# Performance work log

Measured on AMD Instinct MI355X. Metric: run time of the kernel, lower is better.

## Reference

```python
import jax, jax.numpy as jnp
import numpy as np

B, S, IN, EMB, H = 4, 2048, 256, 512, 8
D = EMB // H
SCALE = 1.0 / np.sqrt(EMB)  # source uses 1/sqrt(embed_size), not head_dim
EPS = 1e-5


def setup_inputs() -> dict:
    key = jax.random.key(0)
    ks = jax.random.split(key, 20)
    def w(k, shape, fan_in):
        return jax.random.normal(k, shape, jnp.float32) * (1.0 / np.sqrt(fan_in))
    inp = {"state_emb": jax.random.normal(ks[0], (B, S, IN), jnp.float32)}
    i = 1
    for p in ("q", "k", "v"):
        inp[f"{p}_W1"] = w(ks[i], (IN, EMB), IN); i += 1
        inp[f"{p}_b1"] = jnp.zeros((EMB,), jnp.float32)
        inp[f"{p}_W2"] = w(ks[i], (EMB, EMB), EMB); i += 1
        inp[f"{p}_b2"] = jnp.zeros((EMB,), jnp.float32)
    inp["f_W1"] = w(ks[i], (EMB, 2 * EMB), EMB); i += 1
    inp["f_b1"] = jnp.zeros((2 * EMB,), jnp.float32)
    inp["f_W2"] = w(ks[i], (2 * EMB, EMB), 2 * EMB); i += 1
    inp["f_b2"] = jnp.zeros((EMB,), jnp.float32)
    inp["ln1_g"] = jnp.ones((EMB,), jnp.float32)
    inp["ln1_b"] = jnp.zeros((EMB,), jnp.float32)
    inp["ln2_g"] = jnp.ones((EMB,), jnp.float32)
    inp["ln2_b"] = jnp.zeros((EMB,), jnp.float32)
    return inp


def _mlp2(x, W1, b1, W2, b2):
    return jax.nn.relu(x @ W1 + b1) @ W2 + b2


def _layernorm(x, g, b):
    mu = jnp.mean(x, axis=-1, keepdims=True)
    var = jnp.mean(jnp.square(x - mu), axis=-1, keepdims=True)
    return (x - mu) * jax.lax.rsqrt(var + EPS) * g + b


def reference(state_emb, q_W1, q_b1, q_W2, q_b2, k_W1, k_b1, k_W2, k_b2,
              v_W1, v_b1, v_W2, v_b2, f_W1, f_b1, f_W2, f_b2,
              ln1_g, ln1_b, ln2_g, ln2_b):
    n, dim = state_emb.shape[0], state_emb.shape[1]
    q = _mlp2(state_emb, q_W1, q_b1, q_W2, q_b2)  # [n, dim, EMB]
    k = _mlp2(state_emb, k_W1, k_b1, k_W2, k_b2)
    v = _mlp2(state_emb, v_W1, v_b1, v_W2, v_b2)
    qh = q.reshape(n, dim, H, D)
    kh = k.reshape(n, dim, H, D)
    vh = v.reshape(n, dim, H, D)
    energy = jnp.einsum('nqhd,nkhd->nhqk', qh, kh)  # [n, H, dim, dim]
    attn = jax.nn.softmax(energy * SCALE, axis=-1)
    ctx = jnp.einsum('nhql,nlhd->nqhd', attn, vh).reshape(n, dim, EMB)
    x = _layernorm(ctx + q, ln1_g, ln1_b)  # residual with queries, per source
    ff = _mlp2(x, f_W1, f_b1, f_W2, f_b2)
    return _layernorm(x + ff, ln2_g, ln2_b)
```

## Files before the change

kernel.cpp:

```cpp
#include <hip/hip_runtime.h>
#include <hip/hip_bf16.h>
#include <math.h>

#define BB   4
#define SS   2048
#define INF_ 256
#define EMB  512
#define NH   8
#define HD   64
#define NT   8192

typedef unsigned short u16;
typedef unsigned int   u32;
typedef __attribute__((ext_vector_type(8))) short bf16x8;
typedef __attribute__((ext_vector_type(8))) unsigned short u16x8;
typedef __attribute__((ext_vector_type(4))) float f32x4;

constexpr float C2  = 0.06375871607f;
constexpr float TB  = 1.00390625f;
constexpr float EPS = 1e-5f;

__device__ __forceinline__ u16 f2bf(float v) {
    __hip_bfloat16 h = __float2bfloat16(v);
    return *(u16*)&h;
}
__device__ __forceinline__ float bf2f(u16 u) {
    __hip_bfloat16 h = *(__hip_bfloat16*)&u;
    return __bfloat162float(h);
}
__device__ __forceinline__ u16 ftrunc_bf(float v) {
    return (u16)(__float_as_uint(v * TB) >> 16);
}
__device__ __forceinline__ f32x4 mfma16(bf16x8 a, bf16x8 b, f32x4 c) {
    return __builtin_amdgcn_mfma_f32_16x16x32_bf16(a, b, c, 0, 0, 0);
}
__device__ __forceinline__ void async16(const void* g, void* l) {
    __builtin_amdgcn_global_load_lds(
        (const __attribute__((address_space(1))) void*)g,
        (__attribute__((address_space(3))) void*)l, 16, 0, 0);
}
__device__ __forceinline__ int derive_flag(const u16* x) {
    const int lane = threadIdx.x & 63;
    const unsigned e = (x[lane * 2] >> 7) & 0xFF;
    float pl = (e == 0 || (e >= 110 && e <= 140)) ? 1.0f : 0.0f;
    #pragma unroll
    for (int o = 1; o < 64; o <<= 1) pl += __shfl_xor(pl, o);
    return pl < 32.0f;
}

__global__ __launch_bounds__(256) void prep(
    const u16* __restrict__ xsrc,
    const void* w0, const void* w1, const void* w2, const void* w3,
    const void* w4, const void* w5, const void* w6, const void* w7,
    const void* p0, const void* p1, const void* p2, const void* p3,
    const void* p4, const void* p5, const void* p6, const void* p7,
    const void* p8, const void* p9, const void* p10, const void* p11,
    u16* __restrict__ xbf, u16* __restrict__ wt1, u16* __restrict__ wt2,
    u16* __restrict__ f1t, u16* __restrict__ f2t, float* __restrict__ small)
{
    const int isf = derive_flag(xsrc);
    const int z = blockIdx.z;
    const int tid = threadIdx.x;

    if (z < 8) {
        int K, M; const void* src; u16* dst;
        switch (z) {
            case 0: K=256;  M=512;  src=w0; dst=wt1;             break;
            case 1: K=256;  M=512;  src=w1; dst=wt1+512*256;     break;
            case 2: K=256;  M=512;  src=w2; dst=wt1+2*512*256;   break;
            case 3: K=512;  M=512;  src=w3; dst=wt2;             break;
            case 4: K=512;  M=512;  src=w4; dst=wt2+512*512;     break;
            case 5: K=512;  M=512;  src=w5; dst=wt2+2*512*512;   break;
            case 6: K=512;  M=1024; src=w6; dst=f1t;             break;
            default:K=1024; M=512;  src=w7; dst=f2t;             break;
        }
        const int m0 = blockIdx.x * 32, k0 = blockIdx.y * 32;
        if (m0 >= M || k0 >= K) return;
        __shared__ u16 t[32][33];
        const int tx = tid & 31, ty = tid >> 5;
        #pragma unroll
        for (int i = 0; i < 4; ++i) {
            const int kk = k0 + ty + i * 8;
            t[ty + i * 8][tx] = isf ? ftrunc_bf(((const float*)src)[(size_t)kk * M + m0 + tx])
                                    : ((const u16*)src)[(size_t)kk * M + m0 + tx];
        }
        __syncthreads();
        #pragma unroll
        for (int i = 0; i < 4; ++i) {
            const int mm = m0 + ty + i * 8;
            dst[(size_t)mm * K + k0 + tx] = t[tx][ty + i * 8];
        }
    } else if (z == 8) {
        const int bid = blockIdx.y * 32 + blockIdx.x;
        const int base = bid * 2048 + tid * 8;
        if (isf) {
            #pragma unroll
            for (int j = 0; j < 8; ++j)
                xbf[base + j] = ftrunc_bf(((const float*)xsrc)[base + j]);
        } else {
            *(u16x8*)&xbf[base] = *(const u16x8*)&xsrc[base];
        }
    } else {
        const int bid = blockIdx.y * 32 + blockIdx.x;
        if (bid >= 28) return;
        const int e = bid * 256 + tid;
        int id, i;
        if (e < 3072)      { id = e >> 9;               i = e & 511;          }
        else if (e < 4096) { id = 6;                    i = e - 3072;         }
        else               { id = 7 + ((e - 4096) >> 9); i = (e - 4096) & 511; }
        const void* src;
        switch (id) {
            case 0: src = p0; break;  case 1: src = p1; break;
            case 2: src = p2; break;  case 3: src = p3; break;
            case 4: src = p4; break;  case 5: src = p5; break;
            case 6: src = p6; break;  case 7: src = p7; break;
            case 8: src = p8; break;  case 9: src = p9; break;
            case 10: src = p10; break; default: src = p11; break;
        }
        small[e] = isf ? ((const float*)src)[i] : bf2f(((const u16*)src)[i]);
    }
}

template <bool RELU, bool AWHICH, bool VOUT, bool SCALEK>
__global__ __launch_bounds__(256) void gemm64(
    const u16* __restrict__ Aall, const u16* __restrict__ Wtall,
    const float* __restrict__ ball, u16* __restrict__ out,
    u16* __restrict__ vtb, int N, int K, int M)
{
    __shared__ __align__(16) u16 sA[64 * 64];
    __shared__ __align__(16) u16 sB[64 * 64];

    const int mtiles = M >> 6;
    const int which = blockIdx.y / mtiles;
    const int colb  = blockIdx.y % mtiles;
    const int row0 = blockIdx.x << 6, col0 = colb << 6;
    const u16* A  = Aall + (AWHICH ? (size_t)which * N * K : 0);
    const u16* Wt = Wtall + (size_t)which * M * K;
    const float* bias = ball + (size_t)which * M;

    const int tid = threadIdx.x;
    const int lane = tid & 63, w = tid >> 6;
    const int wrow = (w & 1) << 5, wcol = (w >> 1) << 5;
    const int c = lane & 15, quad = lane >> 4;

    const u16* ap[2]; const u16* bp[2];
    #pragma unroll
    for (int i = 0; i < 2; ++i) {
        const int raw = i * 256 + tid, r = raw >> 3, ch = (raw & 7) ^ (r & 7);
        ap[i] = A + (size_t)(row0 + r) * K + ch * 8;
        bp[i] = Wt + (size_t)(col0 + r) * K + ch * 8;
    }

    f32x4 acc[2][2] = {};

    for (int k0 = 0; k0 < K; k0 += 64) {
        __syncthreads();
        #pragma unroll
        for (int i = 0; i < 2; ++i) {
            async16(ap[i], (char*)sA + (i * 256 + tid) * 16);
            ap[i] += 64;
            async16(bp[i], (char*)sB + (i * 256 + tid) * 16);
            bp[i] += 64;
        }
        __syncthreads();

        #pragma unroll
        for (int kt = 0; kt < 2; ++kt) {
            bf16x8 af[2], bfr[2];
            #pragma unroll
            for (int rt = 0; rt < 2; ++rt) {
                const int r = wrow + rt * 16 + c;
                af[rt] = *(const bf16x8*)&sA[(r * 8 + ((kt * 4 + quad) ^ (r & 7))) * 8];
            }
            #pragma unroll
            for (int ct = 0; ct < 2; ++ct) {
                const int r = wcol + ct * 16 + c;
                bfr[ct] = *(const bf16x8*)&sB[(r * 8 + ((kt * 4 + quad) ^ (r & 7))) * 8];
            }
            #pragma unroll
            for (int rt = 0; rt < 2; ++rt)
                #pragma unroll
                for (int ct = 0; ct < 2; ++ct)
                    acc[rt][ct] = mfma16(af[rt], bfr[ct], acc[rt][ct]);
        }
    }

    if (VOUT && which == 2) {
        __syncthreads();
        #pragma unroll
        for (int rt = 0; rt < 2; ++rt) {
            const int rowb = wrow + rt * 16 + quad * 4;
            #pragma unroll
            for (int ct = 0; ct < 2; ++ct) {
                const int col = wcol + ct * 16 + c;
                const float bb = bias[col0 + col];
                ushort4 pk;
                pk.x = ftrunc_bf(acc[rt][ct][0] + bb);
                pk.y = ftrunc_bf(acc[rt][ct][1] + bb);
                pk.z = ftrunc_bf(acc[rt][ct][2] + bb);
                pk.w = ftrunc_bf(acc[rt][ct][3] + bb);
                *(ushort4*)&sA[col * 72 + rowb] = pk;
            }
        }
        __syncthreads();
        const int dl = tid >> 2, part = tid & 3;
        const int hg = (col0 + dl) >> 6, dd = (col0 + dl) & 63;
        const int bb = row0 >> 11, s0 = row0 & 2047;
        u16* dst = vtb + ((size_t)(bb * NH + hg) * HD + dd) * SS + s0 + part * 16;
        #pragma unroll
        for (int j = 0; j < 2; ++j)
            *(u16x8*)&dst[j * 8] = *(const u16x8*)&sA[dl * 72 + part * 16 + j * 8];
        return;
    }

    const float sc = (SCALEK && which == 1) ? C2 : 1.0f;
    const size_t outW = (size_t)which * N * M;
    #pragma unroll
    for (int rt = 0; rt < 2; ++rt) {
        #pragma unroll
        for (int i = 0; i < 4; ++i) {
            const int row = row0 + wrow + rt * 16 + quad * 4 + i;
            #pragma unroll
            for (int ct = 0; ct < 2; ++ct) {
                const int col = col0 + wcol + ct * 16 + c;
                float v = (acc[rt][ct][i] + bias[col]) * sc;
                if (RELU) v = fmaxf(v, 0.0f);
                out[outW + (size_t)row * M + col] = ftrunc_bf(v);
            }
        }
    }
}

__global__ __launch_bounds__(512) void attn_mfma(
    const u16* __restrict__ q, const u16* __restrict__ k,
    const u16* __restrict__ vt, u16* __restrict__ ctx)
{
    __shared__ __align__(16) u16 sK[2][64 * 64];
    __shared__ __align__(16) u16 sV[2][64 * 64];
    __shared__ __align__(16) u16 sP[8][16 * 64];

    const int tid = threadIdx.x;
    const int w = tid >> 6, lane = tid & 63;
    const int c = lane & 15, quad = lane >> 4;
    const int id = blockIdx.x;
    const int slot = id >> 3;
    const int bh = ((id & 7) << 2) | (slot >> 4);
    const int qt = slot & 15;
    const int b = bh >> 3, h = bh & 7;
    const int q0 = qt * 128;
    const size_t tokbase = (size_t)b * SS;
    const int hoff = h * HD;

    const int myq = q0 + w * 16 + c;
    bf16x8 qf[2];
    #pragma unroll
    for (int kt = 0; kt < 2; ++kt)
        qf[kt] = *(const bf16x8*)&q[(tokbase + myq) * EMB + hoff + kt * 32 + quad * 8];

    union { u32 u[4]; bf16x8 v; } ones;
    #pragma unroll
    for (int i = 0; i < 4; ++i) ones.u[i] = 0x3F803F80u;

    const u16* kp; const u16* vp;
    {
        const int rr = tid >> 3, ch = (tid & 7) ^ (rr & 7);
        kp = k + (tokbase + rr) * EMB + hoff + ch * 8;
        vp = vt + ((size_t)(b * NH + h) * HD + rr) * SS + ch * 8;
    }
    auto stage = [&](int buf) {
        async16(kp, (char*)&sK[buf][0] + tid * 16);
        kp += 64 * EMB;
        async16(vp, (char*)&sV[buf][0] + tid * 16);
        vp += 64;
    };
    stage(0);

    f32x4 accO[4] = {};
    f32x4 accL = {};
    const f32x4 zc = {};

    for (int t = 0; t < SS / 64; ++t) {
        __syncthreads();
        const int buf = t & 1;
        if (t + 1 < SS / 64) stage(buf ^ 1);

        f32x4 accS[4];
        #pragma unroll
        for (int mt = 0; mt < 4; ++mt) {
            const int key = mt * 16 + c;
            bf16x8 kf0 = *(const bf16x8*)&sK[buf][(key * 8 + (quad ^ (key & 7))) * 8];
            accS[mt] = mfma16(kf0, qf[0], zc);
            bf16x8 kf1 = *(const bf16x8*)&sK[buf][(key * 8 + ((4 + quad) ^ (key & 7))) * 8];
            accS[mt] = mfma16(kf1, qf[1], accS[mt]);
        }

        u32 pw[8];
        #pragma unroll
        for (int mt = 0; mt < 4; ++mt) {
            const float e0 = __builtin_amdgcn_exp2f(accS[mt][0]);
            const float e1 = __builtin_amdgcn_exp2f(accS[mt][1]);
            const float e2 = __builtin_amdgcn_exp2f(accS[mt][2]);
            const float e3 = __builtin_amdgcn_exp2f(accS[mt][3]);
            pw[2 * mt]     = __builtin_amdgcn_perm(__float_as_uint(e1), __float_as_uint(e0), 0x07060302u);
            pw[2 * mt + 1] = __builtin_amdgcn_perm(__float_as_uint(e3), __float_as_uint(e2), 0x07060302u);
        }

        #pragma unroll
        for (int mt = 0; mt < 4; ++mt) {
            const int chunkW = 2 * mt + (quad >> 1);
            const int blk = c * 8 + (chunkW ^ (c & 7));
            uint2 u; u.x = pw[2 * mt]; u.y = pw[2 * mt + 1];
            *(uint2*)((char*)&sP[w][0] + blk * 16 + 8 * (quad & 1)) = u;
        }

        bf16x8 pf[2];
        #pragma unroll
        for (int kt = 0; kt < 2; ++kt)
            pf[kt] = *(const bf16x8*)&sP[w][(c * 8 + ((kt * 4 + quad) ^ (c & 7))) * 8];
        accL = mfma16(ones.v, pf[0], accL);
        accL = mfma16(ones.v, pf[1], accL);
        #pragma unroll
        for (int nt = 0; nt < 4; ++nt) {
            const int d = nt * 16 + c;
            #pragma unroll
            for (int kt = 0; kt < 2; ++kt) {
                bf16x8 vf = *(const bf16x8*)&sV[buf][(d * 8 + ((kt * 4 + quad) ^ (d & 7))) * 8];
                accO[nt] = mfma16(vf, pf[kt], accO[nt]);
            }
        }
    }

    const float l = accL[0];
    const float li = (l > 0.0f) ? (1.0f / l) : 0.0f;

    const int tok = q0 + w * 16 + c;
    u16* dst = ctx + (tokbase + tok) * EMB + hoff + quad * 4;
    #pragma unroll
    for (int nt = 0; nt < 4; ++nt) {
        ushort4 pk;
        pk.x = ftrunc_bf(accO[nt][0] * li);
        pk.y = ftrunc_bf(accO[nt][1] * li);
        pk.z = ftrunc_bf(accO[nt][2] * li);
        pk.w = ftrunc_bf(accO[nt][3] * li);
        *(ushort4*)&dst[nt * 16] = pk;
    }
}

__global__ __launch_bounds__(256) void ln_mid(
    const u16* __restrict__ a, const u16* __restrict__ b2,
    const float* __restrict__ g, const float* __restrict__ be,
    u16* __restrict__ outb)
{
    const int wave = threadIdx.x >> 6, lane = threadIdx.x & 63;
    const size_t row = (size_t)blockIdx.x * 4 + wave;
    const u16x8 av = *(const u16x8*)&a[row * EMB + lane * 8];
    const u16x8 bv = *(const u16x8*)&b2[row * EMB + lane * 8];
    float vals[8], sum = 0.0f;
    #pragma unroll
    for (int i = 0; i < 8; ++i) { vals[i] = bf2f(av[i]) + bf2f(bv[i]); sum += vals[i]; }
    #pragma unroll
    for (int o = 1; o < 64; o <<= 1) sum += __shfl_xor(sum, o);
    const float mu = sum * (1.0f / 512.0f);
    float vs = 0.0f;
    #pragma unroll
    for (int i = 0; i < 8; ++i) { const float d = vals[i] - mu; vs += d * d; }
    #pragma unroll
    for (int o = 1; o < 64; o <<= 1) vs += __shfl_xor(vs, o);
    const float rstd = rsqrtf(vs * (1.0f / 512.0f) + EPS);
    u16x8 ov;
    #pragma unroll
    for (int i = 0; i < 8; ++i) {
        const int col = lane * 8 + i;
        ov[i] = f2bf((vals[i] - mu) * rstd * g[col] + be[col]);
    }
    *(u16x8*)&outb[row * EMB + lane * 8] = ov;
}

__global__ __launch_bounds__(256) void ln_final(
    const u16* __restrict__ a, const u16* __restrict__ b2,
    const float* __restrict__ g, const float* __restrict__ be,
    void* __restrict__ dout, const u16* __restrict__ xsrc)
{
    const int isf = derive_flag(xsrc);
    const int wave = threadIdx.x >> 6, lane = threadIdx.x & 63;
    const size_t row = (size_t)blockIdx.x * 4 + wave;
    const u16x8 av = *(const u16x8*)&a[row * EMB + lane * 8];
    const u16x8 bv = *(const u16x8*)&b2[row * EMB + lane * 8];
    float vals[8], sum = 0.0f;
    #pragma unroll
    for (int i = 0; i < 8; ++i) { vals[i] = bf2f(av[i]) + bf2f(bv[i]); sum += vals[i]; }
    #pragma unroll
    for (int o = 1; o < 64; o <<= 1) sum += __shfl_xor(sum, o);
    const float mu = sum * (1.0f / 512.0f);
    float vs = 0.0f;
    #pragma unroll
    for (int i = 0; i < 8; ++i) { const float d = vals[i] - mu; vs += d * d; }
    #pragma unroll
    for (int o = 1; o < 64; o <<= 1) vs += __shfl_xor(vs, o);
    const float rstd = rsqrtf(vs * (1.0f / 512.0f) + EPS);
    if (isf) {
        #pragma unroll
        for (int i = 0; i < 8; ++i) {
            const int col = lane * 8 + i;
            ((float*)dout)[row * EMB + col] = (vals[i] - mu) * rstd * g[col] + be[col];
        }
    } else {
        u16x8 ov;
        #pragma unroll
        for (int i = 0; i < 8; ++i) {
            const int col = lane * 8 + i;
            ov[i] = f2bf((vals[i] - mu) * rstd * g[col] + be[col]);
        }
        *(u16x8*)&((u16*)dout)[row * EMB + lane * 8] = ov;
    }
}

extern "C" void kernel_launch(void* const* d_in, const int* in_sizes, int n_in,
                              void* d_out, int out_size, void* d_ws, size_t ws_size,
                              hipStream_t stream)
{
    char* ws = (char*)d_ws;
    float* small = (float*)(ws + 0);
    u16*   wt1   = (u16*)(ws + 32768);
    u16*   wt2   = (u16*)(ws + 819200);
    u16*   f1t   = (u16*)(ws + 2392064);
    u16*   f2t   = (u16*)(ws + 3440640);
    u16*   xbf   = (u16*)(ws + 4489216);
    u16*   h3    = (u16*)(ws + 8683520);
    u16*   qkv   = (u16*)(ws + 33849344);
    u16*   vtb   = (u16*)(ws + 59015168);
    u16*   ctxb  = (u16*)(ws + 67403776);
    u16*   x1b   = (u16*)(ws + 75792384);
    u16*   ffb   = (u16*)(ws + 84180992);

    const dim3 blk(256);
    const u16* xsrc = (const u16*)d_in[0];

    prep<<<dim3(32, 32, 10), blk, 0, stream>>>(
        xsrc,
        d_in[1], d_in[5], d_in[9], d_in[3], d_in[7], d_in[11], d_in[13], d_in[15],
        d_in[2], d_in[6], d_in[10], d_in[4], d_in[8], d_in[12],
        d_in[14], d_in[16], d_in[17], d_in[18], d_in[19], d_in[20],
        xbf, wt1, wt2, f1t, f2t, small);

    gemm64<true, false, false, false><<<dim3(128, 24), blk, 0, stream>>>(
        xbf, wt1, small + 0, h3, nullptr, NT, INF_, EMB);
    gemm64<false, true, true, true><<<dim3(128, 24), blk, 0, stream>>>(
        h3, wt2, small + 1536, qkv, vtb, NT, EMB, EMB);

    attn_mfma<<<dim3(512), dim3(512), 0, stream>>>(
        qkv, qkv + (size_t)NT * EMB, vtb, ctxb);

    ln_mid<<<NT / 4, blk, 0, stream>>>(ctxb, qkv, small + 4608, small + 5120, x1b);

    u16* h2 = h3;
    gemm64<true, false, false, false><<<dim3(128, 16), blk, 0, stream>>>(
        x1b, f1t, small + 3072, h2, nullptr, NT, EMB, 1024);
    gemm64<false, false, false, false><<<dim3(128, 8), blk, 0, stream>>>(
        h2, f2t, small + 4096, ffb, nullptr, NT, 1024, EMB);

    ln_final<<<NT / 4, blk, 0, stream>>>(x1b, ffb, small + 5632, small + 6144, d_out, xsrc);
}
```

Baseline: 233.5 us.

## Process two query fragments per wave in attention to reuse K/V tiles

Each wave in the attention kernel now handles 32 queries (two 16-row fragments) instead of 16. The block covers 256 queries and the grid is halved to 256 blocks. Every K and V fragment read from LDS, and every global K/V tile staged, now feeds twice as many MFMAs, which cuts LDS traffic and redundant K/V loads. In exchange it doubles accumulator registers and the per-wave P scratch in shared memory. It also leaves only 256 blocks, which may underfill the 256 CUs and lowers occupancy.

Measured after the change: 245.8 us. 5.3% more time.

```diff
diff --git a/kernel.cpp b/kernel.cpp
--- a/kernel.cpp
+++ b/kernel.cpp
@@ -237,25 +237,28 @@
 {
     __shared__ __align__(16) u16 sK[2][64 * 64];
     __shared__ __align__(16) u16 sV[2][64 * 64];
-    __shared__ __align__(16) u16 sP[8][16 * 64];
+    __shared__ __align__(16) u16 sP[16][16 * 64];
 
     const int tid = threadIdx.x;
     const int w = tid >> 6, lane = tid & 63;
     const int c = lane & 15, quad = lane >> 4;
     const int id = blockIdx.x;
     const int slot = id >> 3;
-    const int bh = ((id & 7) << 2) | (slot >> 4);
-    const int qt = slot & 15;
+    const int bh = ((id & 7) << 2) | (slot >> 3);
+    const int qt = slot & 7;
     const int b = bh >> 3, h = bh & 7;
-    const int q0 = qt * 128;
+    const int q0 = qt * 256;
     const size_t tokbase = (size_t)b * SS;
     const int hoff = h * HD;
 
-    const int myq = q0 + w * 16 + c;
-    bf16x8 qf[2];
-    #pragma unroll
-    for (int kt = 0; kt < 2; ++kt)
-        qf[kt] = *(const bf16x8*)&q[(tokbase + myq) * EMB + hoff + kt * 32 + quad * 8];
+    bf16x8 qf[2][2];
+    #pragma unroll
+    for (int f = 0; f < 2; ++f) {
+        const int myq = q0 + w * 32 + f * 16 + c;
+        #pragma unroll
+        for (int kt = 0; kt < 2; ++kt)
+            qf[f][kt] = *(const bf16x8*)&q[(tokbase + myq) * EMB + hoff + kt * 32 + quad * 8];
+    }
 
     union { u32 u[4]; bf16x8 v; } ones;
     #pragma unroll
@@ -275,8 +278,8 @@
     };
     stage(0);
 
-    f32x4 accO[4] = {};
-    f32x4 accL = {};
+    f32x4 accO[2][4] = {};
+    f32x4 accL[2] = {};
     const f32x4 zc = {};
 
     for (int t = 0; t < SS / 64; ++t) {
@@ -284,65 +287,78 @@
         const int buf = t & 1;
         if (t + 1 < SS / 64) stage(buf ^ 1);
 
-        f32x4 accS[4];
+        f32x4 accS[2][4];
         #pragma unroll
         for (int mt = 0; mt < 4; ++mt) {
             const int key = mt * 16 + c;
             bf16x8 kf0 = *(const bf16x8*)&sK[buf][(key * 8 + (quad ^ (key & 7))) * 8];
-            accS[mt] = mfma16(kf0, qf[0], zc);
+            #pragma unroll
+            for (int f = 0; f < 2; ++f)
+                accS[f][mt] = mfma16(kf0, qf[f][0], zc);
             bf16x8 kf1 = *(const bf16x8*)&sK[buf][(key * 8 + ((4 + quad) ^ (key & 7))) * 8];
-            accS[mt] = mfma16(kf1, qf[1], accS[mt]);
-        }
-
-        u32 pw[8];
-        #pragma unroll
-        for (int mt = 0; mt < 4; ++mt) {
-            const float e0 = __builtin_amdgcn_exp2f(accS[mt][0]);
-            const float e1 = __builtin_amdgcn_exp2f(accS[mt][1]);
-            const float e2 = __builtin_amdgcn_exp2f(accS[mt][2]);
-            const float e3 = __builtin_amdgcn_exp2f(accS[mt][3]);
-            pw[2 * mt]     = __builtin_amdgcn_perm(__float_as_uint(e1), __float_as_uint(e0), 0x07060302u);
-            pw[2 * mt + 1] = __builtin_amdgcn_perm(__float_as_uint(e3), __float_as_uint(e2), 0x07060302u);
-        }
-
-        #pragma unroll
-        for (int mt = 0; mt < 4; ++mt) {
-            const int chunkW = 2 * mt + (quad >> 1);
-            const int blk = c * 8 + (chunkW ^ (c & 7));
-            uint2 u; u.x = pw[2 * mt]; u.y = pw[2 * mt + 1];
-            *(uint2*)((char*)&sP[w][0] + blk * 16 + 8 * (quad & 1)) = u;
-        }
-
-        bf16x8 pf[2];
-        #pragma unroll
-        for (int kt = 0; kt < 2; ++kt)
-            pf[kt] = *(const bf16x8*)&sP[w][(c * 8 + ((kt * 4 + quad) ^ (c & 7))) * 8];
-        accL = mfma16(ones.v, pf[0], accL);
-        accL = mfma16(ones.v, pf[1], accL);
+            #pragma unroll
+            for (int f = 0; f < 2; ++f)
+                accS[f][mt] = mfma16(kf1, qf[f][1], accS[f][mt]);
+        }
+
+        #pragma unroll
+        for (int f = 0; f < 2; ++f) {
+            u32 pw[8];
+            #pragma unroll
+            for (int mt = 0; mt < 4; ++mt) {
+                const float e0 = __builtin_amdgcn_exp2f(accS[f][mt][0]);
+                const float e1 = __builtin_amdgcn_exp2f(accS[f][mt][1]);
+                const float e2 = __builtin_amdgcn_exp2f(accS[f][mt][2]);
+                const float e3 = __builtin_amdgcn_exp2f(accS[f][mt][3]);
+                pw[2 * mt]     = __builtin_amdgcn_perm(__float_as_uint(e1), __float_as_uint(e0), 0x07060302u);
+                pw[2 * mt + 1] = __builtin_amdgcn_perm(__float_as_uint(e3), __float_as_uint(e2), 0x07060302u);
+            }
+            #pragma unroll
+            for (int mt = 0; mt < 4; ++mt) {
+                const int chunkW = 2 * mt + (quad >> 1);
+                const int blk = c * 8 + (chunkW ^ (c & 7));
+                uint2 u; u.x = pw[2 * mt]; u.y = pw[2 * mt + 1];
+                *(uint2*)((char*)&sP[w * 2 + f][0] + blk * 16 + 8 * (quad & 1)) = u;
+            }
+        }
+
+        bf16x8 pf[2][2];
+        #pragma unroll
+        for (int f = 0; f < 2; ++f) {
+            #pragma unroll
+            for (int kt = 0; kt < 2; ++kt)
+                pf[f][kt] = *(const bf16x8*)&sP[w * 2 + f][(c * 8 + ((kt * 4 + quad) ^ (c & 7))) * 8];
+            accL[f] = mfma16(ones.v, pf[f][0], accL[f]);
+            accL[f] = mfma16(ones.v, pf[f][1], accL[f]);
+        }
         #pragma unroll
         for (int nt = 0; nt < 4; ++nt) {
             const int d = nt * 16 + c;
             #pragma unroll
             for (int kt = 0; kt < 2; ++kt) {
                 bf16x8 vf = *(const bf16x8*)&sV[buf][(d * 8 + ((kt * 4 + quad) ^ (d & 7))) * 8];
-                accO[nt] = mfma16(vf, pf[kt], accO[nt]);
-            }
-        }
-    }
-
-    const float l = accL[0];
-    const float li = (l > 0.0f) ? (1.0f / l) : 0.0f;
-
-    const int tok = q0 + w * 16 + c;
-    u16* dst = ctx + (tokbase + tok) * EMB + hoff + quad * 4;
-    #pragma unroll
-    for (int nt = 0; nt < 4; ++nt) {
-        ushort4 pk;
-        pk.x = ftrunc_bf(accO[nt][0] * li);
-        pk.y = ftrunc_bf(accO[nt][1] * li);
-        pk.z = ftrunc_bf(accO[nt][2] * li);
-        pk.w = ftrunc_bf(accO[nt][3] * li);
-        *(ushort4*)&dst[nt * 16] = pk;
+                #pragma unroll
+                for (int f = 0; f < 2; ++f)
+                    accO[f][nt] = mfma16(vf, pf[f][kt], accO[f][nt]);
+            }
+        }
+    }
+
+    #pragma unroll
+    for (int f = 0; f < 2; ++f) {
+        const float l = accL[f][0];
+        const float li = (l > 0.0f) ? (1.0f / l) : 0.0f;
+        const int tok = q0 + w * 32 + f * 16 + c;
+        u16* dst = ctx + (tokbase + tok) * EMB + hoff + quad * 4;
+        #pragma unroll
+        for (int nt = 0; nt < 4; ++nt) {
+            ushort4 pk;
+            pk.x = ftrunc_bf(accO[f][nt][0] * li);
+            pk.y = ftrunc_bf(accO[f][nt][1] * li);
+            pk.z = ftrunc_bf(accO[f][nt][2] * li);
+            pk.w = ftrunc_bf(accO[f][nt][3] * li);
+            *(ushort4*)&dst[nt * 16] = pk;
+        }
     }
 }
 
@@ -448,7 +464,7 @@
     gemm64<false, true, true, true><<<dim3(128, 24), blk, 0, stream>>>(
         h3, wt2, small + 1536, qkv, vtb, NT, EMB, EMB);
 
-    attn_mfma<<<dim3(512), dim3(512), 0, stream>>>(
+    attn_mfma<<<dim3(256), dim3(512), 0, stream>>>(
         qkv, qkv + (size_t)NT * EMB, vtb, ctxb);
 
     ln_mid<<<NT / 4, blk, 0, stream>>>(ctxb, qkv, small + 4608, small + 5120, x1b);
```
